# Kernel tuning notes

Measured on AMD Instinct MI355X. Metric: run time of the kernel, lower is better.

## Reference

```python
import jax, jax.numpy as jnp
import numpy as np


def setup_inputs() -> dict:
    key = jax.random.key(0)
    k1, k2, k3, k4 = jax.random.split(key, 4)
    N, E, D, B = 50000, 100000, 64, 16
    atom_features = jax.random.normal(k1, (N, D), dtype=jnp.float32)
    bond_features = jax.random.normal(k2, (E, B), dtype=jnp.float32)
    pair_indices = jax.random.randint(k3, (E, 2), 0, N, dtype=jnp.int32)
    kernel = jax.random.normal(k4, (B, D * D), dtype=jnp.float32) * (1.0 / np.sqrt(B))
    bias = jnp.zeros((D * D,), dtype=jnp.float32)
    return {
        "atom_features": atom_features,
        "bond_features": bond_features,
        "pair_indices": pair_indices,
        "kernel": kernel,
        "bias": bias,
    }


def reference(atom_features, bond_features, pair_indices, kernel, bias):
    N, D = atom_features.shape
    # Per-edge transformation matrix: [E, D, D]
    edge_mat = (bond_features @ kernel + bias).reshape(-1, D, D)
    # Gather neighbor atom features: [E, D]
    neighbors = atom_features[pair_indices[:, 1]]
    # Per-edge matvec (matmul with expand/squeeze in original): [E, D]
    transformed = jnp.einsum("eij,ej->ei", edge_mat, neighbors)
    # Scatter-add into destination atoms: [N, D]
    aggregated = jax.ops.segment_sum(transformed, pair_indices[:, 0], num_segments=N)
    return aggregated
```

## Files before the change

### kernel.cpp

```cpp
#include <hip/hip_runtime.h>

typedef _Float16 half8  __attribute__((ext_vector_type(8)));
typedef _Float16 half2v __attribute__((ext_vector_type(2)));
typedef float    f32x4  __attribute__((ext_vector_type(4)));

#define BB 16
#define NB_B 17
#define BM 64
#define PACK_BLKS 34
#define ZERO_BLKS 1024

__device__ __forceinline__ void gll16(const void* g, void* l) {
  __builtin_amdgcn_global_load_lds(
      (const __attribute__((address_space(1))) void*)g,
      (__attribute__((address_space(3))) void*)l, 16, 0, 0);
}

__global__ void prep(const float* __restrict__ kern, const float* __restrict__ bias,
                     _Float16* __restrict__ ktg, f32x4* __restrict__ out4, int n4) {
  if (blockIdx.x < PACK_BLKS) {
    int g = blockIdx.x * 256 + threadIdx.x;
    int s = g >> 8, t = (g >> 6) & 3, l = g & 63;
    int i = t * 16 + (l & 15);
    int k0 = s * 32 + (l >> 4) * 8;
    _Float16 v[8];
#pragma unroll
    for (int e = 0; e < 8; ++e) {
      int k = k0 + e, b = k >> 6, j = k & 63;
      float x = (b < BB) ? kern[b * 4096 + i * 64 + j] : bias[i * 64 + j];
      v[e] = (_Float16)x;
    }
    size_t dst = (size_t)(s >> 1) * 4096 + (size_t)(s & 1) * 2048 + t * 512 + l * 8;
    *(half8*)(ktg + dst) = *(const half8*)v;
  } else {
    int i = (blockIdx.x - PACK_BLKS) * 256 + threadIdx.x;
    for (; i < n4; i += ZERO_BLKS * 256) out4[i] = (f32x4){0.f, 0.f, 0.f, 0.f};
  }
}

__global__ __launch_bounds__(256, 5)
void edge_gemm(const float* __restrict__ atom, const float* __restrict__ bond,
               const int* __restrict__ pair, const _Float16* __restrict__ ktg,
               float* __restrict__ out, int E) {
  __shared__ __align__(16) _Float16 nb[BM * 64];
  __shared__ __align__(16) char bbuf[2][8192];
  __shared__ _Float16 bndh[NB_B * BM];
  __shared__ int srcs[BM];
  __shared__ int nbrs[BM];

  const int tid = threadIdx.x;
  const int e0  = blockIdx.x * BM;

  if (tid < BM) {
    const int e = e0 + tid;
    const bool valid = e < E;
    int2 p2 = valid ? *(const int2*)(pair + 2 * e) : (int2){0, 0};
    srcs[tid] = p2.x;
    nbrs[tid] = p2.y;
  }
  gll16((const char*)ktg + tid * 16,        (char*)bbuf[0] + tid * 16);
  gll16((const char*)ktg + 4096 + tid * 16, (char*)bbuf[0] + 4096 + tid * 16);
  __syncthreads();

  if (tid < BM) {
    const int e = e0 + tid;
    const bool valid = e < E;
    const f32x4* brow = (const f32x4*)(bond + (size_t)e * BB);
#pragma unroll
    for (int q = 0; q < 4; ++q) {
      f32x4 bv = {0.f, 0.f, 0.f, 0.f};
      if (valid) bv = brow[q];
#pragma unroll
      for (int z = 0; z < 4; ++z) bndh[(q * 4 + z) * BM + tid] = (_Float16)bv[z];
    }
    bndh[16 * BM + tid] = valid ? (_Float16)1.0f : (_Float16)0.0f;
  }

#pragma unroll
  for (int it = 0; it < 2; ++it) {
    const int idx = it * 256 + tid;
    const int r = idx >> 3, c8 = idx & 7;
    const int nbr = nbrs[r];
    const bool valid = (e0 + r) < E;
    f32x4 x0 = {0.f,0.f,0.f,0.f}, x1 = {0.f,0.f,0.f,0.f};
    if (valid) {
      const f32x4* arow = (const f32x4*)(atom + (size_t)nbr * 64);
      x0 = arow[2 * c8]; x1 = arow[2 * c8 + 1];
    }
    _Float16 h[8];
    h[0] = (_Float16)x0[0]; h[1] = (_Float16)x0[1]; h[2] = (_Float16)x0[2]; h[3] = (_Float16)x0[3];
    h[4] = (_Float16)x1[0]; h[5] = (_Float16)x1[1]; h[6] = (_Float16)x1[2]; h[7] = (_Float16)x1[3];
    *(half8*)((char*)nb + r * 128 + ((c8 ^ (r & 7)) << 4)) = *(const half8*)h;
  }
  __syncthreads();

  const int lane = tid & 63, wave = tid >> 6;
  const int wm = wave >> 1, wn = wave & 1;
  const int l15 = lane & 15, lg = lane >> 4;

  half8 a[2][2];
#pragma unroll
  for (int t = 0; t < 2; ++t) {
    const int r = wm * 32 + t * 16 + l15;
    const int rb = r * 128, sw = (r & 7) << 4;
#pragma unroll
    for (int p = 0; p < 2; ++p)
      a[t][p] = *(const half8*)((const char*)nb + rb + (((p * 4 + lg) << 4) ^ sw));
  }

  f32x4 acc[2][2];
#pragma unroll
  for (int t = 0; t < 2; ++t)
#pragma unroll
    for (int n = 0; n < 2; ++n) acc[t][n] = (f32x4){0.f, 0.f, 0.f, 0.f};

  for (int b = 0; b < NB_B; ++b) {
    if (b + 1 < NB_B) {
      const char* src = (const char*)ktg + (size_t)(b + 1) * 8192;
      char* dst = (char*)bbuf[(b + 1) & 1];
      gll16(src + tid * 16,        dst + tid * 16);
      gll16(src + 4096 + tid * 16, dst + 4096 + tid * 16);
    }
    const _Float16 s0 = bndh[b * BM + wm * 32 + l15];
    const _Float16 s1 = bndh[b * BM + wm * 32 + 16 + l15];
    const half2v sc0 = {s0, s0}, sc1 = {s1, s1};
    const char* bp = (const char*)bbuf[b & 1] + (size_t)(wn * 2) * 1024 + lane * 16;
#pragma unroll
    for (int sp = 0; sp < 2; ++sp) {
      half8 a0 = a[0][sp], a1 = a[1][sp];
      half2v* a0p = (half2v*)&a0; half2v* a1p = (half2v*)&a1;
#pragma unroll
      for (int q = 0; q < 4; ++q) { a0p[q] = a0p[q] * sc0; a1p[q] = a1p[q] * sc1; }
#pragma unroll
      for (int nt = 0; nt < 2; ++nt) {
        const half8 bf = *(const half8*)(bp + sp * 4096 + nt * 1024);
        acc[0][nt] = __builtin_amdgcn_mfma_f32_16x16x32_f16(a0, bf, acc[0][nt], 0, 0, 0);
        acc[1][nt] = __builtin_amdgcn_mfma_f32_16x16x32_f16(a1, bf, acc[1][nt], 0, 0, 0);
      }
    }
    __syncthreads();
  }

#pragma unroll
  for (int t = 0; t < 2; ++t) {
#pragma unroll
    for (int rr = 0; rr < 4; ++rr) {
      const int el = wm * 32 + t * 16 + lg * 4 + rr;
      if (e0 + el < E) {
        float* dst = out + (size_t)srcs[el] * 64 + wn * 32 + l15;
        atomicAdd(dst,      acc[t][0][rr]);
        atomicAdd(dst + 16, acc[t][1][rr]);
      }
    }
  }
}

extern "C" void kernel_launch(void* const* d_in, const int* in_sizes, int n_in,
                              void* d_out, int out_size, void* d_ws, size_t ws_size,
                              hipStream_t stream) {
  const float* atom = (const float*)d_in[0];
  const float* bond = (const float*)d_in[1];
  const int*   pair = (const int*)d_in[2];
  const float* kern = (const float*)d_in[3];
  const float* bias = (const float*)d_in[4];
  float* out = (float*)d_out;
  _Float16* ktg = (_Float16*)d_ws;

  const int E  = in_sizes[1] / BB;
  const int n4 = out_size / 4;

  prep<<<PACK_BLKS + ZERO_BLKS, 256, 0, stream>>>(kern, bias, ktg, (f32x4*)out, n4);
  edge_gemm<<<(E + BM - 1) / BM, 256, 0, stream>>>(atom, bond, pair, ktg, out, E);
}
```

Baseline: 109.1 us.

## Replace float atomic scatter with per-destination linked lists and gather kernel

Instead of atomically adding each edge's result into the output, the edge kernel writes per-edge results to a workspace buffer and builds per-destination linked lists with atomicExch. A new gather kernel walks each node's list with one wave per node and writes the output directly, so the output no longer needs zero-filling. The kernel weights are permuted so each lane writes two adjacent floats. This trades float atomics for an extra 25.6MB write/read round trip, pointer-chasing latency in the gather, and a third launch.

```diff
diff --git a/kernel.cpp b/kernel.cpp
--- a/kernel.cpp
+++ b/kernel.cpp
@@ -3,12 +3,18 @@
 typedef _Float16 half8  __attribute__((ext_vector_type(8)));
 typedef _Float16 half2v __attribute__((ext_vector_type(2)));
 typedef float    f32x4  __attribute__((ext_vector_type(4)));
+typedef float    f32x2  __attribute__((ext_vector_type(2)));
+typedef int      i32x4  __attribute__((ext_vector_type(4)));
 
 #define BB 16
 #define NB_B 17
 #define BM 64
 #define PACK_BLKS 34
-#define ZERO_BLKS 1024
+#define INIT_BLKS 64
+
+#define TRANS_OFF (1u << 20)
+#define HEAD_OFF  (28u << 20)
+#define NEXT_OFF  (29u << 20)
 
 __device__ __forceinline__ void gll16(const void* g, void* l) {
   __builtin_amdgcn_global_load_lds(
@@ -17,11 +23,11 @@
 }
 
 __global__ void prep(const float* __restrict__ kern, const float* __restrict__ bias,
-                     _Float16* __restrict__ ktg, f32x4* __restrict__ out4, int n4) {
+                     _Float16* __restrict__ ktg, int* __restrict__ head, int n4head) {
   if (blockIdx.x < PACK_BLKS) {
     int g = blockIdx.x * 256 + threadIdx.x;
     int s = g >> 8, t = (g >> 6) & 3, l = g & 63;
-    int i = t * 16 + (l & 15);
+    int i = (t >> 1) * 32 + 2 * (l & 15) + (t & 1);
     int k0 = s * 32 + (l >> 4) * 8;
     _Float16 v[8];
 #pragma unroll
@@ -33,19 +39,20 @@
     size_t dst = (size_t)(s >> 1) * 4096 + (size_t)(s & 1) * 2048 + t * 512 + l * 8;
     *(half8*)(ktg + dst) = *(const half8*)v;
   } else {
+    i32x4* h4 = (i32x4*)head;
     int i = (blockIdx.x - PACK_BLKS) * 256 + threadIdx.x;
-    for (; i < n4; i += ZERO_BLKS * 256) out4[i] = (f32x4){0.f, 0.f, 0.f, 0.f};
+    for (; i < n4head; i += INIT_BLKS * 256) h4[i] = (i32x4){-1, -1, -1, -1};
   }
 }
 
 __global__ __launch_bounds__(256, 5)
 void edge_gemm(const float* __restrict__ atom, const float* __restrict__ bond,
                const int* __restrict__ pair, const _Float16* __restrict__ ktg,
-               float* __restrict__ out, int E) {
+               float* __restrict__ trans, int* __restrict__ head,
+               int* __restrict__ next, int E) {
   __shared__ __align__(16) _Float16 nb[BM * 64];
   __shared__ __align__(16) char bbuf[2][8192];
   __shared__ _Float16 bndh[NB_B * BM];
-  __shared__ int srcs[BM];
   __shared__ int nbrs[BM];
 
   const int tid = threadIdx.x;
@@ -55,8 +62,8 @@
     const int e = e0 + tid;
     const bool valid = e < E;
     int2 p2 = valid ? *(const int2*)(pair + 2 * e) : (int2){0, 0};
-    srcs[tid] = p2.x;
     nbrs[tid] = p2.y;
+    if (valid) next[e] = atomicExch(&head[p2.x], e);
   }
   gll16((const char*)ktg + tid * 16,        (char*)bbuf[0] + tid * 16);
   gll16((const char*)ktg + 4096 + tid * 16, (char*)bbuf[0] + 4096 + tid * 16);
@@ -147,11 +154,27 @@
     for (int rr = 0; rr < 4; ++rr) {
       const int el = wm * 32 + t * 16 + lg * 4 + rr;
       if (e0 + el < E) {
-        float* dst = out + (size_t)srcs[el] * 64 + wn * 32 + l15;
-        atomicAdd(dst,      acc[t][0][rr]);
-        atomicAdd(dst + 16, acc[t][1][rr]);
+        f32x2 v = {acc[t][0][rr], acc[t][1][rr]};
+        *(f32x2*)(trans + (size_t)(e0 + el) * 64 + wn * 32 + 2 * l15) = v;
       }
     }
+  }
+}
+
+__global__ __launch_bounds__(256)
+void gather(const float* __restrict__ trans, const int* __restrict__ head,
+            const int* __restrict__ next, float* __restrict__ out, int N) {
+  const int lane = threadIdx.x & 63;
+  const int w    = (blockIdx.x * blockDim.x + threadIdx.x) >> 6;
+  const int nw   = (gridDim.x * blockDim.x) >> 6;
+  for (int n = w; n < N; n += nw) {
+    float acc = 0.f;
+    int e = head[n];
+    while (e >= 0) {
+      acc += trans[(size_t)e * 64 + lane];
+      e = next[e];
+    }
+    out[(size_t)n * 64 + lane] = acc;
   }
 }
 
@@ -164,11 +187,18 @@
   const float* kern = (const float*)d_in[3];
   const float* bias = (const float*)d_in[4];
   float* out = (float*)d_out;
-  _Float16* ktg = (_Float16*)d_ws;
-
-  const int E  = in_sizes[1] / BB;
-  const int n4 = out_size / 4;
-
-  prep<<<PACK_BLKS + ZERO_BLKS, 256, 0, stream>>>(kern, bias, ktg, (f32x4*)out, n4);
-  edge_gemm<<<(E + BM - 1) / BM, 256, 0, stream>>>(atom, bond, pair, ktg, out, E);
-}
+
+  _Float16* ktg  = (_Float16*)d_ws;
+  float*    trans = (float*)((char*)d_ws + TRANS_OFF);
+  int*      head  = (int*)((char*)d_ws + HEAD_OFF);
+  int*      next  = (int*)((char*)d_ws + NEXT_OFF);
+
+  const int E = in_sizes[1] / BB;
+  const int N = out_size / 64;
+  const int n4head = (N + 3) / 4;
+
+  prep<<<PACK_BLKS + INIT_BLKS, 256, 0, stream>>>(kern, bias, ktg, head, n4head);
+  edge_gemm<<<(E + BM - 1) / BM, 256, 0, stream>>>(atom, bond, pair, ktg,
+                                                   trans, head, next, E);
+  gather<<<1024, 256, 0, stream>>>(trans, head, next, out, N);
+}
```

After: 117.4 us. 7.6% more time.
